# Performance work log

Measured on AMD Instinct MI355X. Metric: run time of the kernel, lower is better.

The kernel has to match this reference:

```python
import jax, jax.numpy as jnp
import numpy as np
import math

N_CELLS = 16384
INPUT_DIM = 512
HIDDEN = 512


def build_neighbors(n):
    n_bits = max(1, int(math.ceil(math.log2(n))))
    idx = np.arange(n)
    flips = [idx ^ (1 << b) for b in range(n_bits)]
    ring = [(idx + 1) % n, (idx - 1) % n]
    allnb = np.stack(flips + ring, axis=1)
    # dedupe per row; for power-of-2 n every row has exactly n_bits+1 uniques
    rows = [sorted(set(r.tolist())) for r in allnb]
    return np.asarray(rows, dtype=np.int32)


def setup_inputs() -> dict:
    key = jax.random.key(0)
    ks = jax.random.split(key, 12)
    n, d, h = N_CELLS, INPUT_DIM, HIDDEN
    amp = jax.random.uniform(ks[0], (n, h)) * 0.5 + 0.5
    phase = jax.random.normal(ks[1], (n, h)) * 0.3 + (2 * math.pi * jnp.arange(n) / n)[:, None]
    return {
        "x": jax.random.normal(ks[2], (1, d), dtype=jnp.float32),
        "pump_W": jax.random.normal(ks[3], (n, d), dtype=jnp.float32) / np.sqrt(d),
        "pump_b": jax.random.normal(ks[4], (n,), dtype=jnp.float32) * 0.01,
        "dec_W": jax.random.normal(ks[5], (d, 2 * h), dtype=jnp.float32) / np.sqrt(2 * h),
        "dec_b": jax.random.normal(ks[6], (d,), dtype=jnp.float32) * 0.01,
        "cs_re": (amp * jnp.cos(phase)).astype(jnp.float32),
        "cs_im": (amp * jnp.sin(phase)).astype(jnp.float32),
        "excited": jax.random.uniform(ks[7], (n,)) * 0.6,  # some cells above 0.5 threshold
        "phase_vel": jax.random.normal(ks[8], (n, h), dtype=jnp.float32) * 0.05,
        "cav_re": jax.random.normal(ks[9], (h,), dtype=jnp.float32) * 0.01,
        "cav_im": jax.random.normal(ks[10], (h,), dtype=jnp.float32) * 0.01,
        "neighbors": jnp.asarray(build_neighbors(n)),
    }


def reference(x, pump_W, pump_b, dec_W, dec_b, cs_re, cs_im, excited, phase_vel, cav_re, cav_im, neighbors):
    states = (cs_re + 1j * cs_im).astype(jnp.complex64)          # [n,h]
    cavity = (cav_re + 1j * cav_im).astype(jnp.complex64)        # [h]

    # pump + excited fraction update
    pump = jax.nn.sigmoid(x @ pump_W.T + pump_b)[0]              # [n]
    excited = jnp.clip(excited * 0.95 + pump * 0.05, 0.0, 1.0)

    # free phase rotation: polar(1, 0.1*phase_vel)
    states = states * jnp.exp(1j * (phase_vel * 0.1)).astype(jnp.complex64)

    # neighbor phase coupling (hypercube + ring, k=15 neighbors each)
    ang = jnp.angle(states)                                      # [n,h]
    nb_states = states[neighbors]                                # [n,k,h]
    coupling = jnp.cos(ang[:, None, :] - ang[neighbors])         # [n,k,h]
    interference = 0.1 * jnp.sum(coupling * nb_states, axis=1)   # [n,h]
    k = neighbors.shape[1]
    new_states = 0.7 * states + 0.3 * interference / k

    # lasing: population inversion threshold
    lasing = excited > 0.5                                       # [n]
    n_lasing = jnp.sum(lasing)
    maskf = lasing.astype(jnp.float32)[:, None]
    # emission uses pre-phase-lock states (torch copies lasing_cells first)
    emission = jnp.sum(new_states * maskf, axis=0) / jnp.maximum(n_lasing, 1).astype(jnp.float32)
    cavity_new = jnp.where(n_lasing > 0, 0.8 * cavity + 0.2 * emission, cavity)

    # phase-lock lasing cells to (old) cavity phase
    cavity_phase = jnp.angle(cavity)                             # old cavity
    new_ang = jnp.angle(new_states)
    locked = 0.3 * cavity_phase[None, :] + 0.7 * new_ang
    locked_states = jnp.abs(new_states) * jnp.exp(1j * locked)
    new_states = jnp.where(lasing[:, None], locked_states.astype(jnp.complex64), new_states)
    excited = jnp.where(lasing, excited * 0.9, excited * 0.98)

    # cavity feedback (updated cavity) + amplitude renorm
    new_states = new_states + 0.05 * cavity_new[None, :]
    amp = jnp.abs(new_states)
    amp = amp / (jnp.max(amp, axis=-1, keepdims=True) + 1e-8)
    final_states = (amp * jnp.exp(1j * jnp.angle(new_states))).astype(jnp.complex64)

    # decode cavity mode
    out_real = jnp.concatenate([cavity_new.real, cavity_new.imag])[None, :].astype(jnp.float32)  # [1,2h]
    pred = out_real @ dec_W.T + dec_b                            # [1, input_dim]
    tension = jnp.var(jnp.abs(final_states))
    return pred, tension
```

## Files before the change

### kernel.cpp

```cpp
#include <hip/hip_runtime.h>
#include <hip/hip_fp16.h>
#include <math.h>

#define N_CELLS 16384
#define HID 512
#define IND 512
#define KNB 15
#define NCOPY 64

#define ROT_BLOCKS  8192
#define PUMP_BLOCKS 4096
#define ZERO_BLOCKS 64

#define EMIS_OFF  128
#define LAS_OFF   (EMIS_OFF + NCOPY*1024*4)
#define CAV_OFF   (LAS_OFF + N_CELLS*4)
#define VPART_OFF (CAV_OFF + 1536*4)
#define ROT_OFF   (1<<20)
#define NST_OFF   (ROT_OFF + (size_t)N_CELLS*HID*4)

__device__ inline __half2 f2h2(float f) { union { float f; __half2 h; } u; u.f = f; return u.h; }
__device__ inline float   h22f(__half2 h) { union { float f; __half2 h; } u; u.h = h; return u.f; }

__global__ __launch_bounds__(256) void k_front(const float* __restrict__ cr,
                                               const float* __restrict__ ci,
                                               const float* __restrict__ pv,
                                               __half2* __restrict__ rot,
                                               const float* __restrict__ x,
                                               const float* __restrict__ pW,
                                               const float* __restrict__ pb,
                                               const float* __restrict__ excited,
                                               int* __restrict__ lasing,
                                               float* __restrict__ emis) {
    int b = blockIdx.x;
    int tid = threadIdx.x;
    if (b < ROT_BLOCKS) {
        int i = b * 256 + tid;
        const float4* cr4 = (const float4*)cr;
        const float4* ci4 = (const float4*)ci;
        const float4* pv4 = (const float4*)pv;
        float4 a = cr4[i], bb = ci4[i], t = pv4[i];
        float s0, c0, s1, c1, s2, c2, s3, c3;
        __sincosf(0.1f * t.x, &s0, &c0);
        __sincosf(0.1f * t.y, &s1, &c1);
        __sincosf(0.1f * t.z, &s2, &c2);
        __sincosf(0.1f * t.w, &s3, &c3);
        __half2 p0 = __floats2half2_rn(a.x * c0 - bb.x * s0, a.x * s0 + bb.x * c0);
        __half2 p1 = __floats2half2_rn(a.y * c1 - bb.y * s1, a.y * s1 + bb.y * c1);
        __half2 p2 = __floats2half2_rn(a.z * c2 - bb.z * s2, a.z * s2 + bb.z * c2);
        __half2 p3 = __floats2half2_rn(a.w * c3 - bb.w * s3, a.w * s3 + bb.w * c3);
        ((float4*)rot)[i] = make_float4(h22f(p0), h22f(p1), h22f(p2), h22f(p3));
    } else if (b < ROT_BLOCKS + PUMP_BLOCKS) {
        int gtid = (b - ROT_BLOCKS) * 256 + tid;
        int cell = gtid >> 6;
        int lane = gtid & 63;
        const float4* w4 = (const float4*)(pW + (size_t)cell * IND);
        const float4* x4 = (const float4*)x;
        float acc = 0.f;
#pragma unroll
        for (int t = 0; t < (IND / 4) / 64; ++t) {
            float4 a = w4[lane + 64 * t];
            float4 bx = x4[lane + 64 * t];
            acc += a.x * bx.x + a.y * bx.y + a.z * bx.z + a.w * bx.w;
        }
#pragma unroll
        for (int o = 32; o; o >>= 1) acc += __shfl_xor(acc, o, 64);
        if (lane == 0) {
            float p = 1.f / (1.f + expf(-(acc + pb[cell])));
            float e = excited[cell] * 0.95f + p * 0.05f;
            e = fminf(fmaxf(e, 0.f), 1.f);
            lasing[cell] = (e > 0.5f) ? 1 : 0;
        }
    } else {
        int idx = (b - ROT_BLOCKS - PUMP_BLOCKS) * 256 + tid;
        ((float4*)emis)[idx] = make_float4(0.f, 0.f, 0.f, 0.f);
    }
}

__global__ __launch_bounds__(256) void k_coup(const __half2* __restrict__ rot,
                                              const int* __restrict__ nbrs,
                                              const int* __restrict__ lasing,
                                              __half2* __restrict__ nst,
                                              float* __restrict__ emis) {
    __shared__ int nb[KNB];
    __shared__ int las;
    int cell = blockIdx.x;
    int tid = threadIdx.x;
    if (tid < KNB) nb[tid] = nbrs[cell * KNB + tid];
    if (tid == KNB) las = lasing[cell];
    __syncthreads();

    const float2* rot2 = (const float2*)rot;
    float2 raw = rot2[(size_t)cell * (HID / 2) + tid];
    __half2 sa = f2h2(raw.x), sb = f2h2(raw.y);
    __half2 sre = __halves2half2(__low2half(sa), __low2half(sb));
    __half2 sim = __halves2half2(__high2half(sa), __high2half(sb));
    float s0x = __low2float(sa), s0y = __high2float(sa);
    float s1x = __low2float(sb), s1y = __high2float(sb);
    float r0 = rsqrtf(s0x * s0x + s0y * s0y);
    float r1 = rsqrtf(s1x * s1x + s1y * s1y);

    __half2 are = __float2half2_rn(0.f), aim = __float2half2_rn(0.f);
#pragma unroll
    for (int t = 0; t < KNB; ++t) {
        float2 qraw = rot2[(size_t)nb[t] * (HID / 2) + tid];
        __half2 qa = f2h2(qraw.x), qb = f2h2(qraw.y);
        __half2 qre = __halves2half2(__low2half(qa), __low2half(qb));
        __half2 qim = __halves2half2(__high2half(qa), __high2half(qb));
        __half2 d  = __hfma2(sim, qim, __hmul2(sre, qre));
        __half2 qn = __hfma2(qim, qim, __hmul2(qre, qre));
        __half2 t2 = __hmul2(d, h2rsqrt(qn));
        are = __hfma2(t2, qre, are);
        aim = __hfma2(t2, qim, aim);
    }
    float ar0 = __low2float(are), ar1 = __high2float(are);
    float ai0 = __low2float(aim), ai1 = __high2float(aim);
    float k0 = 0.002f * r0, k1 = 0.002f * r1;
    float nr0 = 0.7f * s0x + k0 * ar0, ni0 = 0.7f * s0y + k0 * ai0;
    float nr1 = 0.7f * s1x + k1 * ar1, ni1 = 0.7f * s1y + k1 * ai1;
    float2 st = make_float2(h22f(__floats2half2_rn(nr0, ni0)),
                            h22f(__floats2half2_rn(nr1, ni1)));
    ((float2*)nst)[(size_t)cell * (HID / 2) + tid] = st;
    if (las) {
        int c0 = tid << 1;
        float* em = emis + (size_t)(cell & (NCOPY - 1)) * 1024;
        atomicAdd(em + c0,     nr0); atomicAdd(em + 512 + c0,     ni0);
        atomicAdd(em + c0 + 1, nr1); atomicAdd(em + 512 + c0 + 1, ni1);
    }
}

__global__ __launch_bounds__(512) void k_cav(const float* __restrict__ emis,
                                             const int* __restrict__ lasv,
                                             const float* __restrict__ cavr,
                                             const float* __restrict__ cavi,
                                             float* __restrict__ cav) {
    __shared__ int cnt[8];
    __shared__ int snl;
    int c = threadIdx.x;
    int wid = c >> 6, lane = c & 63;
    const int4* l4 = (const int4*)lasv;
    int n = 0;
#pragma unroll
    for (int k = 0; k < N_CELLS / 4 / 512; ++k) {
        int4 v = l4[c + 512 * k];
        n += v.x + v.y + v.z + v.w;
    }
#pragma unroll
    for (int o = 32; o; o >>= 1) n += __shfl_xor(n, o, 64);
    if (lane == 0) cnt[wid] = n;
    __syncthreads();
    if (c == 0) { int t = 0; for (int k = 0; k < 8; ++k) t += cnt[k]; snl = t; }
    __syncthreads();
    int nl = snl;

    float er = 0.f, ei = 0.f;
#pragma unroll 8
    for (int k = 0; k < NCOPY; ++k) {
        er += emis[k * 1024 + c];
        ei += emis[k * 1024 + 512 + c];
    }
    float cr = cavr[c], ci = cavi[c];
    float nr, ni;
    if (nl > 0) {
        float inv = 1.f / (float)(nl > 1 ? nl : 1);
        nr = 0.8f * cr + 0.2f * er * inv;
        ni = 0.8f * ci + 0.2f * ei * inv;
    } else {
        nr = cr;
        ni = ci;
    }
    cav[c] = nr;
    cav[512 + c] = ni;
    cav[1024 + c] = atan2f(ci, cr);
}

__global__ __launch_bounds__(512) void k_pred(const float* __restrict__ cav,
                                              const float* __restrict__ dW,
                                              const float* __restrict__ db,
                                              float* __restrict__ out) {
    int gtid = blockIdx.x * 512 + threadIdx.x;
    int j = gtid >> 6;
    int lane = gtid & 63;
    const float4* w4 = (const float4*)(dW + (size_t)j * (2 * HID));
    const float4* o4 = (const float4*)cav;
    float acc = 0.f;
#pragma unroll
    for (int t = 0; t < (2 * HID / 4) / 64; ++t) {
        float4 a = w4[lane + 64 * t];
        float4 b = o4[lane + 64 * t];
        acc += a.x * b.x + a.y * b.y + a.z * b.z + a.w * b.w;
    }
#pragma unroll
    for (int o = 32; o; o >>= 1) acc += __shfl_xor(acc, o, 64);
    if (lane == 0) out[j] = acc + db[j];
}

__global__ __launch_bounds__(512) void k_fin(const __half2* __restrict__ nst,
                                             const int* __restrict__ lasing,
                                             const float* __restrict__ cav,
                                             float2* __restrict__ vpart) {
    __shared__ float sred[8];
    __shared__ float sbc;
    int cell = blockIdx.x;
    int c = threadIdx.x;
    int wid = c >> 6, lane = c & 63;
    int las = lasing[cell];

    __half2 vh = nst[(size_t)cell * HID + c];
    float vx = __low2float(vh), vy = __high2float(vh);
    if (las) {
        float r = sqrtf(vx * vx + vy * vy);
        float ang = atan2f(vy, vx);
        float locked = 0.3f * cav[1024 + c] + 0.7f * ang;
        float sn, cs;
        __sincosf(locked, &sn, &cs);
        vx = r * cs; vy = r * sn;
    }
    vx += 0.05f * cav[c];
    vy += 0.05f * cav[512 + c];
    float amp = sqrtf(vx * vx + vy * vy);

    float m = amp;
#pragma unroll
    for (int o = 32; o; o >>= 1) m = fmaxf(m, __shfl_xor(m, o, 64));
    if (lane == 0) sred[wid] = m;
    __syncthreads();
    if (c == 0) {
        float mm = sred[0];
        for (int k = 1; k < 8; ++k) mm = fmaxf(mm, sred[k]);
        sbc = mm;
    }
    __syncthreads();
    float a = amp / (sbc + 1e-8f);

    float s1 = a, s2 = a * a;
#pragma unroll
    for (int o = 32; o; o >>= 1) { s1 += __shfl_xor(s1, o, 64); s2 += __shfl_xor(s2, o, 64); }
    __shared__ float w1[8], w2[8];
    if (lane == 0) { w1[wid] = s1; w2[wid] = s2; }
    __syncthreads();
    if (c == 0) {
        float t1 = 0.f, t2 = 0.f;
        for (int k = 0; k < 8; ++k) { t1 += w1[k]; t2 += w2[k]; }
        vpart[cell] = make_float2(t1, t2);
    }
}

__global__ __launch_bounds__(1024) void k_var(const float2* __restrict__ vpart,
                                              float* __restrict__ out) {
    __shared__ double l1[16], l2[16];
    int c = threadIdx.x;
    int wid = c >> 6, lane = c & 63;
    double s1 = 0.0, s2 = 0.0;
#pragma unroll
    for (int t = 0; t < N_CELLS / 1024; ++t) {
        float2 p = vpart[c + 1024 * t];
        s1 += (double)p.x;
        s2 += (double)p.y;
    }
#pragma unroll
    for (int o = 32; o; o >>= 1) { s1 += __shfl_xor(s1, o, 64); s2 += __shfl_xor(s2, o, 64); }
    if (lane == 0) { l1[wid] = s1; l2[wid] = s2; }
    __syncthreads();
    if (c == 0) {
        double t1 = 0.0, t2 = 0.0;
        for (int k = 0; k < 16; ++k) { t1 += l1[k]; t2 += l2[k]; }
        double n = (double)N_CELLS * (double)HID;
        double mean = t1 / n;
        out[IND] = (float)(t2 / n - mean * mean);
    }
}

extern "C" void kernel_launch(void* const* d_in, const int* in_sizes, int n_in,
                              void* d_out, int out_size, void* d_ws, size_t ws_size,
                              hipStream_t stream) {
    const float* x       = (const float*)d_in[0];
    const float* pump_W  = (const float*)d_in[1];
    const float* pump_b  = (const float*)d_in[2];
    const float* dec_W   = (const float*)d_in[3];
    const float* dec_b   = (const float*)d_in[4];
    const float* cs_re   = (const float*)d_in[5];
    const float* cs_im   = (const float*)d_in[6];
    const float* excited = (const float*)d_in[7];
    const float* pvel    = (const float*)d_in[8];
    const float* cav_re  = (const float*)d_in[9];
    const float* cav_im  = (const float*)d_in[10];
    const int*   nbrs    = (const int*)d_in[11];

    float* out = (float*)d_out;
    char* ws = (char*)d_ws;
    float*   emis  = (float*)(ws + EMIS_OFF);
    int*     lasv  = (int*)(ws + LAS_OFF);
    float*   cav   = (float*)(ws + CAV_OFF);
    float2*  vpart = (float2*)(ws + VPART_OFF);
    __half2* rot   = (__half2*)(ws + ROT_OFF);
    __half2* nst   = (__half2*)(ws + NST_OFF);

    k_front<<<ROT_BLOCKS + PUMP_BLOCKS + ZERO_BLOCKS, 256, 0, stream>>>(
        cs_re, cs_im, pvel, rot, x, pump_W, pump_b, excited, lasv, emis);
    k_coup<<<N_CELLS, 256, 0, stream>>>(rot, nbrs, lasv, nst, emis);
    k_cav<<<1, 512, 0, stream>>>(emis, lasv, cav_re, cav_im, cav);
    k_pred<<<64, 512, 0, stream>>>(cav, dec_W, dec_b, out);
    k_fin<<<N_CELLS, 512, 0, stream>>>(nst, lasv, cav, vpart);
    k_var<<<1, 1024, 0, stream>>>(vpart, out);
}
```

Baseline: 268.4 us.

## Fuse cavity with decode, fold variance into fin via last-block, repack half layout

Merges the single-block cavity update and the decode matvec into one 64-block kernel in which each block recomputes the cavity into shared memory. The final variance reduction moves into k_fin using an atomic counter and last-block-done pattern, so the k_var launch is removed. Rotated and new states are repacked as separate real/imag half2 pairs, which removes half shuffles in the coupling loop, and k_fin now uses 256 threads handling two elements each. This cuts two kernel launches and some per-element repacking, at the cost of the cavity computation being repeated across 64 blocks and an extra atomic and fence per cell block.

New measurement: 569.0 us. 112% more time.

```diff
diff --git a/kernel.cpp b/kernel.cpp
--- a/kernel.cpp
+++ b/kernel.cpp
@@ -12,6 +12,7 @@
 #define PUMP_BLOCKS 4096
 #define ZERO_BLOCKS 64
 
+#define CNT_OFF   0
 #define EMIS_OFF  128
 #define LAS_OFF   (EMIS_OFF + NCOPY*1024*4)
 #define CAV_OFF   (LAS_OFF + N_CELLS*4)
@@ -25,13 +26,14 @@
 __global__ __launch_bounds__(256) void k_front(const float* __restrict__ cr,
                                                const float* __restrict__ ci,
                                                const float* __restrict__ pv,
-                                               __half2* __restrict__ rot,
+                                               float4* __restrict__ rot,
                                                const float* __restrict__ x,
                                                const float* __restrict__ pW,
                                                const float* __restrict__ pb,
                                                const float* __restrict__ excited,
                                                int* __restrict__ lasing,
-                                               float* __restrict__ emis) {
+                                               float* __restrict__ emis,
+                                               int* __restrict__ cnt) {
     int b = blockIdx.x;
     int tid = threadIdx.x;
     if (b < ROT_BLOCKS) {
@@ -45,11 +47,14 @@
         __sincosf(0.1f * t.y, &s1, &c1);
         __sincosf(0.1f * t.z, &s2, &c2);
         __sincosf(0.1f * t.w, &s3, &c3);
-        __half2 p0 = __floats2half2_rn(a.x * c0 - bb.x * s0, a.x * s0 + bb.x * c0);
-        __half2 p1 = __floats2half2_rn(a.y * c1 - bb.y * s1, a.y * s1 + bb.y * c1);
-        __half2 p2 = __floats2half2_rn(a.z * c2 - bb.z * s2, a.z * s2 + bb.z * c2);
-        __half2 p3 = __floats2half2_rn(a.w * c3 - bb.w * s3, a.w * s3 + bb.w * c3);
-        ((float4*)rot)[i] = make_float4(h22f(p0), h22f(p1), h22f(p2), h22f(p3));
+        float re0 = a.x * c0 - bb.x * s0, im0 = a.x * s0 + bb.x * c0;
+        float re1 = a.y * c1 - bb.y * s1, im1 = a.y * s1 + bb.y * c1;
+        float re2 = a.z * c2 - bb.z * s2, im2 = a.z * s2 + bb.z * c2;
+        float re3 = a.w * c3 - bb.w * s3, im3 = a.w * s3 + bb.w * c3;
+        rot[i] = make_float4(h22f(__floats2half2_rn(re0, re1)),
+                             h22f(__floats2half2_rn(im0, im1)),
+                             h22f(__floats2half2_rn(re2, re3)),
+                             h22f(__floats2half2_rn(im2, im3)));
     } else if (b < ROT_BLOCKS + PUMP_BLOCKS) {
         int gtid = (b - ROT_BLOCKS) * 256 + tid;
         int cell = gtid >> 6;
@@ -72,15 +77,17 @@
             lasing[cell] = (e > 0.5f) ? 1 : 0;
         }
     } else {
-        int idx = (b - ROT_BLOCKS - PUMP_BLOCKS) * 256 + tid;
+        int zb = b - ROT_BLOCKS - PUMP_BLOCKS;
+        int idx = zb * 256 + tid;
         ((float4*)emis)[idx] = make_float4(0.f, 0.f, 0.f, 0.f);
-    }
-}
-
-__global__ __launch_bounds__(256) void k_coup(const __half2* __restrict__ rot,
+        if (zb == 0 && tid == 0) *cnt = 0;
+    }
+}
+
+__global__ __launch_bounds__(256) void k_coup(const float2* __restrict__ rot2,
                                               const int* __restrict__ nbrs,
                                               const int* __restrict__ lasing,
-                                              __half2* __restrict__ nst,
+                                              float2* __restrict__ nst2,
                                               float* __restrict__ emis) {
     __shared__ int nb[KNB];
     __shared__ int las;
@@ -90,13 +97,10 @@
     if (tid == KNB) las = lasing[cell];
     __syncthreads();
 
-    const float2* rot2 = (const float2*)rot;
     float2 raw = rot2[(size_t)cell * (HID / 2) + tid];
-    __half2 sa = f2h2(raw.x), sb = f2h2(raw.y);
-    __half2 sre = __halves2half2(__low2half(sa), __low2half(sb));
-    __half2 sim = __halves2half2(__high2half(sa), __high2half(sb));
-    float s0x = __low2float(sa), s0y = __high2float(sa);
-    float s1x = __low2float(sb), s1y = __high2float(sb);
+    __half2 sre = f2h2(raw.x), sim = f2h2(raw.y);
+    float s0x = __low2float(sre), s1x = __high2float(sre);
+    float s0y = __low2float(sim), s1y = __high2float(sim);
     float r0 = rsqrtf(s0x * s0x + s0y * s0y);
     float r1 = rsqrtf(s1x * s1x + s1y * s1y);
 
@@ -104,9 +108,7 @@
 #pragma unroll
     for (int t = 0; t < KNB; ++t) {
         float2 qraw = rot2[(size_t)nb[t] * (HID / 2) + tid];
-        __half2 qa = f2h2(qraw.x), qb = f2h2(qraw.y);
-        __half2 qre = __halves2half2(__low2half(qa), __low2half(qb));
-        __half2 qim = __halves2half2(__high2half(qa), __high2half(qb));
+        __half2 qre = f2h2(qraw.x), qim = f2h2(qraw.y);
         __half2 d  = __hfma2(sim, qim, __hmul2(sre, qre));
         __half2 qn = __hfma2(qim, qim, __hmul2(qre, qre));
         __half2 t2 = __hmul2(d, h2rsqrt(qn));
@@ -118,9 +120,9 @@
     float k0 = 0.002f * r0, k1 = 0.002f * r1;
     float nr0 = 0.7f * s0x + k0 * ar0, ni0 = 0.7f * s0y + k0 * ai0;
     float nr1 = 0.7f * s1x + k1 * ar1, ni1 = 0.7f * s1y + k1 * ai1;
-    float2 st = make_float2(h22f(__floats2half2_rn(nr0, ni0)),
-                            h22f(__floats2half2_rn(nr1, ni1)));
-    ((float2*)nst)[(size_t)cell * (HID / 2) + tid] = st;
+    nst2[(size_t)cell * (HID / 2) + tid] =
+        make_float2(h22f(__floats2half2_rn(nr0, nr1)),
+                    h22f(__floats2half2_rn(ni0, ni1)));
     if (las) {
         int c0 = tid << 1;
         float* em = emis + (size_t)(cell & (NCOPY - 1)) * 1024;
@@ -129,15 +131,20 @@
     }
 }
 
-__global__ __launch_bounds__(512) void k_cav(const float* __restrict__ emis,
-                                             const int* __restrict__ lasv,
-                                             const float* __restrict__ cavr,
-                                             const float* __restrict__ cavi,
-                                             float* __restrict__ cav) {
+__global__ __launch_bounds__(512) void k_predcav(const float* __restrict__ emis,
+                                                 const int* __restrict__ lasv,
+                                                 const float* __restrict__ cavr,
+                                                 const float* __restrict__ cavi,
+                                                 const float* __restrict__ dW,
+                                                 const float* __restrict__ db,
+                                                 float* __restrict__ cav,
+                                                 float* __restrict__ out) {
+    __shared__ float sout[1024];
     __shared__ int cnt[8];
     __shared__ int snl;
     int c = threadIdx.x;
     int wid = c >> 6, lane = c & 63;
+
     const int4* l4 = (const int4*)lasv;
     int n = 0;
 #pragma unroll
@@ -159,115 +166,121 @@
         er += emis[k * 1024 + c];
         ei += emis[k * 1024 + 512 + c];
     }
-    float cr = cavr[c], ci = cavi[c];
+    float crv = cavr[c], civ = cavi[c];
     float nr, ni;
     if (nl > 0) {
         float inv = 1.f / (float)(nl > 1 ? nl : 1);
-        nr = 0.8f * cr + 0.2f * er * inv;
-        ni = 0.8f * ci + 0.2f * ei * inv;
+        nr = 0.8f * crv + 0.2f * er * inv;
+        ni = 0.8f * civ + 0.2f * ei * inv;
     } else {
-        nr = cr;
-        ni = ci;
-    }
-    cav[c] = nr;
-    cav[512 + c] = ni;
-    cav[1024 + c] = atan2f(ci, cr);
-}
-
-__global__ __launch_bounds__(512) void k_pred(const float* __restrict__ cav,
-                                              const float* __restrict__ dW,
-                                              const float* __restrict__ db,
-                                              float* __restrict__ out) {
-    int gtid = blockIdx.x * 512 + threadIdx.x;
-    int j = gtid >> 6;
-    int lane = gtid & 63;
+        nr = crv;
+        ni = civ;
+    }
+    sout[c] = nr;
+    sout[512 + c] = ni;
+    if (blockIdx.x == 0) {
+        cav[c] = nr;
+        cav[512 + c] = ni;
+        cav[1024 + c] = atan2f(civ, crv);
+    }
+    __syncthreads();
+
+    int j = blockIdx.x * 8 + wid;
     const float4* w4 = (const float4*)(dW + (size_t)j * (2 * HID));
-    const float4* o4 = (const float4*)cav;
+    const float4* o4 = (const float4*)sout;
     float acc = 0.f;
 #pragma unroll
-    for (int t = 0; t < (2 * HID / 4) / 64; ++t) {
+    for (int t = 0; t < 4; ++t) {
         float4 a = w4[lane + 64 * t];
-        float4 b = o4[lane + 64 * t];
-        acc += a.x * b.x + a.y * b.y + a.z * b.z + a.w * b.w;
+        float4 bx = o4[lane + 64 * t];
+        acc += a.x * bx.x + a.y * bx.y + a.z * bx.z + a.w * bx.w;
     }
 #pragma unroll
     for (int o = 32; o; o >>= 1) acc += __shfl_xor(acc, o, 64);
     if (lane == 0) out[j] = acc + db[j];
 }
 
-__global__ __launch_bounds__(512) void k_fin(const __half2* __restrict__ nst,
+__global__ __launch_bounds__(256) void k_fin(const float2* __restrict__ nst2,
                                              const int* __restrict__ lasing,
                                              const float* __restrict__ cav,
-                                             float2* __restrict__ vpart) {
-    __shared__ float sred[8];
+                                             float2* __restrict__ vpart,
+                                             int* __restrict__ cnt,
+                                             float* __restrict__ out) {
+    __shared__ float sred[4];
     __shared__ float sbc;
+    __shared__ float w1[4], w2[4];
     int cell = blockIdx.x;
-    int c = threadIdx.x;
-    int wid = c >> 6, lane = c & 63;
+    int t = threadIdx.x;
+    int wid = t >> 6, lane = t & 63;
     int las = lasing[cell];
-
-    __half2 vh = nst[(size_t)cell * HID + c];
-    float vx = __low2float(vh), vy = __high2float(vh);
+    int c0 = t << 1;
+
+    float2 raw = nst2[(size_t)cell * (HID / 2) + t];
+    __half2 reh = f2h2(raw.x), imh = f2h2(raw.y);
+    float vx0 = __low2float(reh), vx1 = __high2float(reh);
+    float vy0 = __low2float(imh), vy1 = __high2float(imh);
     if (las) {
-        float r = sqrtf(vx * vx + vy * vy);
-        float ang = atan2f(vy, vx);
-        float locked = 0.3f * cav[1024 + c] + 0.7f * ang;
-        float sn, cs;
-        __sincosf(locked, &sn, &cs);
-        vx = r * cs; vy = r * sn;
-    }
-    vx += 0.05f * cav[c];
-    vy += 0.05f * cav[512 + c];
-    float amp = sqrtf(vx * vx + vy * vy);
-
-    float m = amp;
+        float r0 = sqrtf(vx0 * vx0 + vy0 * vy0);
+        float r1 = sqrtf(vx1 * vx1 + vy1 * vy1);
+        float l0 = 0.3f * cav[1024 + c0]     + 0.7f * atan2f(vy0, vx0);
+        float l1 = 0.3f * cav[1024 + c0 + 1] + 0.7f * atan2f(vy1, vx1);
+        float sn0, cs0, sn1, cs1;
+        __sincosf(l0, &sn0, &cs0);
+        __sincosf(l1, &sn1, &cs1);
+        vx0 = r0 * cs0; vy0 = r0 * sn0;
+        vx1 = r1 * cs1; vy1 = r1 * sn1;
+    }
+    vx0 += 0.05f * cav[c0];     vy0 += 0.05f * cav[512 + c0];
+    vx1 += 0.05f * cav[c0 + 1]; vy1 += 0.05f * cav[512 + c0 + 1];
+    float amp0 = sqrtf(vx0 * vx0 + vy0 * vy0);
+    float amp1 = sqrtf(vx1 * vx1 + vy1 * vy1);
+
+    float m = fmaxf(amp0, amp1);
 #pragma unroll
     for (int o = 32; o; o >>= 1) m = fmaxf(m, __shfl_xor(m, o, 64));
     if (lane == 0) sred[wid] = m;
     __syncthreads();
-    if (c == 0) {
-        float mm = sred[0];
-        for (int k = 1; k < 8; ++k) mm = fmaxf(mm, sred[k]);
-        sbc = mm;
-    }
-    __syncthreads();
-    float a = amp / (sbc + 1e-8f);
-
-    float s1 = a, s2 = a * a;
+    if (t == 0)
+        sbc = fmaxf(fmaxf(sred[0], sred[1]), fmaxf(sred[2], sred[3]));
+    __syncthreads();
+    float inv = 1.f / (sbc + 1e-8f);
+    float a0 = amp0 * inv, a1 = amp1 * inv;
+
+    float s1 = a0 + a1, s2 = a0 * a0 + a1 * a1;
 #pragma unroll
     for (int o = 32; o; o >>= 1) { s1 += __shfl_xor(s1, o, 64); s2 += __shfl_xor(s2, o, 64); }
-    __shared__ float w1[8], w2[8];
     if (lane == 0) { w1[wid] = s1; w2[wid] = s2; }
     __syncthreads();
-    if (c == 0) {
-        float t1 = 0.f, t2 = 0.f;
-        for (int k = 0; k < 8; ++k) { t1 += w1[k]; t2 += w2[k]; }
-        vpart[cell] = make_float2(t1, t2);
-    }
-}
-
-__global__ __launch_bounds__(1024) void k_var(const float2* __restrict__ vpart,
-                                              float* __restrict__ out) {
-    __shared__ double l1[16], l2[16];
-    int c = threadIdx.x;
-    int wid = c >> 6, lane = c & 63;
-    double s1 = 0.0, s2 = 0.0;
-#pragma unroll
-    for (int t = 0; t < N_CELLS / 1024; ++t) {
-        float2 p = vpart[c + 1024 * t];
-        s1 += (double)p.x;
-        s2 += (double)p.y;
-    }
-#pragma unroll
-    for (int o = 32; o; o >>= 1) { s1 += __shfl_xor(s1, o, 64); s2 += __shfl_xor(s2, o, 64); }
-    if (lane == 0) { l1[wid] = s1; l2[wid] = s2; }
-    __syncthreads();
-    if (c == 0) {
-        double t1 = 0.0, t2 = 0.0;
-        for (int k = 0; k < 16; ++k) { t1 += l1[k]; t2 += l2[k]; }
-        double n = (double)N_CELLS * (double)HID;
-        double mean = t1 / n;
-        out[IND] = (float)(t2 / n - mean * mean);
+    __shared__ int slast;
+    if (t == 0) {
+        vpart[cell] = make_float2(w1[0] + w1[1] + w1[2] + w1[3],
+                                  w2[0] + w2[1] + w2[2] + w2[3]);
+        __threadfence();
+        int old = atomicAdd(cnt, 1);
+        slast = (old == N_CELLS - 1) ? 1 : 0;
+    }
+    __syncthreads();
+    if (slast) {
+        __threadfence();
+        double d1 = 0.0, d2 = 0.0;
+#pragma unroll
+        for (int k = 0; k < N_CELLS / 256; ++k) {
+            float2 p = vpart[t + 256 * k];
+            d1 += (double)p.x;
+            d2 += (double)p.y;
+        }
+#pragma unroll
+        for (int o = 32; o; o >>= 1) { d1 += __shfl_xor(d1, o, 64); d2 += __shfl_xor(d2, o, 64); }
+        __shared__ double l1[4], l2[4];
+        if (lane == 0) { l1[wid] = d1; l2[wid] = d2; }
+        __syncthreads();
+        if (t == 0) {
+            double t1 = l1[0] + l1[1] + l1[2] + l1[3];
+            double t2 = l2[0] + l2[1] + l2[2] + l2[3];
+            double nn = (double)N_CELLS * (double)HID;
+            double mean = t1 / nn;
+            out[IND] = (float)(t2 / nn - mean * mean);
+        }
     }
 }
 
@@ -289,18 +302,17 @@
 
     float* out = (float*)d_out;
     char* ws = (char*)d_ws;
-    float*   emis  = (float*)(ws + EMIS_OFF);
-    int*     lasv  = (int*)(ws + LAS_OFF);
-    float*   cav   = (float*)(ws + CAV_OFF);
-    float2*  vpart = (float2*)(ws + VPART_OFF);
-    __half2* rot   = (__half2*)(ws + ROT_OFF);
-    __half2* nst   = (__half2*)(ws + NST_OFF);
+    int*    cnt   = (int*)(ws + CNT_OFF);
+    float*  emis  = (float*)(ws + EMIS_OFF);
+    int*    lasv  = (int*)(ws + LAS_OFF);
+    float*  cav   = (float*)(ws + CAV_OFF);
+    float2* vpart = (float2*)(ws + VPART_OFF);
+    float2* rot2  = (float2*)(ws + ROT_OFF);
+    float2* nst2  = (float2*)(ws + NST_OFF);
 
     k_front<<<ROT_BLOCKS + PUMP_BLOCKS + ZERO_BLOCKS, 256, 0, stream>>>(
-        cs_re, cs_im, pvel, rot, x, pump_W, pump_b, excited, lasv, emis);
-    k_coup<<<N_CELLS, 256, 0, stream>>>(rot, nbrs, lasv, nst, emis);
-    k_cav<<<1, 512, 0, stream>>>(emis, lasv, cav_re, cav_im, cav);
-    k_pred<<<64, 512, 0, stream>>>(cav, dec_W, dec_b, out);
-    k_fin<<<N_CELLS, 512, 0, stream>>>(nst, lasv, cav, vpart);
-    k_var<<<1, 1024, 0, stream>>>(vpart, out);
-}
+        cs_re, cs_im, pvel, (float4*)rot2, x, pump_W, pump_b, excited, lasv, emis, cnt);
+    k_coup<<<N_CELLS, 256, 0, stream>>>(rot2, nbrs, lasv, nst2, emis);
+    k_predcav<<<64, 512, 0, stream>>>(emis, lasv, cav_re, cav_im, dec_W, dec_b, cav, out);
+    k_fin<<<N_CELLS, 256, 0, stream>>>(nst2, lasv, cav, vpart, cnt, out);
+}
```
